# Performance work log

Measured on AMD Instinct MI355X. Metric: run time of the kernel, lower is better.

Reference implementation:

```python
import jax, jax.numpy as jnp
import numpy as np

E_NUM, R_NUM, DIM = 100000, 16, 32
BATCH, MAX_STEP, NEIGH, RULES = 1024, 2, 16, 8


def setup_inputs() -> dict:
    key = jax.random.key(0)
    ks = jax.random.split(key, 8)
    users = jax.random.randint(ks[0], (BATCH,), 0, E_NUM)
    items = jax.random.randint(ks[1], (BATCH,), 0, E_NUM)
    rules = jax.random.randint(ks[2], (RULES, MAX_STEP), 0, R_NUM)
    adj = jax.random.randint(ks[3], (R_NUM + 1, E_NUM, NEIGH), 0, E_NUM).astype(jnp.int32)
    ent_embed = jax.random.normal(ks[4], (E_NUM, DIM), jnp.float32) * 0.1
    rule_w = jax.random.normal(ks[5], (RULES,), jnp.float32) * 0.5
    W = jax.random.normal(ks[6], (DIM, 2 * DIM), jnp.float32) * (1.0 / np.sqrt(2 * DIM))
    b = jnp.zeros((DIM,), jnp.float32)
    return dict(users=users, items=items, rules=rules, adj=adj,
                ent_embed=ent_embed, rule_w=rule_w, W=W, b=b)


def _renorm(v, eps=1e-7):
    # emulate nn.Embedding(max_norm=1.0): clip row norms to <= 1 at lookup time
    n = jnp.linalg.norm(v, axis=-1, keepdims=True)
    return v * jnp.minimum(1.0, 1.0 / jnp.maximum(n, eps))


def reference(users, items, rules, adj, ent_embed, rule_w, W, b):
    B = users.shape[0]
    R, S = rules.shape
    N = adj.shape[2]
    dim = ent_embed.shape[1]

    # --- gather entity ids per hop: hop k has [B, R, N^k] (rule-major, as np.hstack) ---
    cur = jnp.broadcast_to(users[:, None], (B, R)).reshape(B, R, 1)
    hops = [cur.reshape(B, -1)]
    for s in range(S):
        rid = rules[:, s]                       # [R] relation id per rule at this step
        nxt = adj[rid[None, :, None], cur]      # [B, R, K, N]
        cur = nxt.reshape(B, R, -1)
        hops.append(cur.reshape(B, -1))

    # --- embed + max_norm renorm ---
    vecs = [_renorm(ent_embed[h]) for h in hops]  # hop k: [B, R*N^k, dim]

    # --- concat aggregator across hops (dropout p=0) ---
    for i in range(S):
        act = jnp.tanh if i == S - 1 else jax.nn.relu
        nxt_vecs = []
        for hop in range(S - i):
            selfv = vecs[hop]                                # [B, M, dim]
            neigh = vecs[hop + 1].reshape(B, -1, N, dim)     # [B, M, N, dim]
            h = jnp.concatenate([selfv, neigh.mean(axis=2)], axis=-1)  # [B, M, 2*dim]
            nxt_vecs.append(act(jnp.einsum('bmd,od->bmo', h, W) + b))
        vecs = nxt_vecs

    res = vecs[0].reshape(B, R, dim)             # per-rule user representation
    rw = _renorm(rule_w[None, :])[0]             # rule_embed with max_norm=1.0
    user_out = jnp.sum(res * rw[None, :, None], axis=1)      # [B, dim]
    item_emb = _renorm(ent_embed[items])                     # [B, dim]
    return jax.nn.sigmoid(jnp.sum(user_out * item_emb, axis=-1))  # [B]
```

## Files before the change

### kernel.cpp

```cpp
#include <hip/hip_runtime.h>
#include <hip/hip_fp16.h>
#include <math.h>

#define E_NUMC 100000
#define DIMC 32
#define NEIGHC 16
#define RULESC 8

struct __align__(16) h2x4 { __half2 x, y, z, w; };
struct __align__(8)  h2x2 { __half2 x, y; };

typedef _Float16 half8 __attribute__((ext_vector_type(8)));
typedef float    floatx4 __attribute__((ext_vector_type(4)));
typedef float    fx2 __attribute__((ext_vector_type(2)));

__global__ __launch_bounds__(256) void renorm_kernel(
    const float* __restrict__ emb, short* __restrict__ o8,
    const float* __restrict__ W, _Float16* __restrict__ Whg)
{
    if (blockIdx.x == 0) {
        const float4* W4 = (const float4*)W;
        const int o = threadIdx.x >> 3, oct = threadIdx.x & 7;
        const float4 wa = W4[o * 16 + 2 * oct];
        const float4 wb = W4[o * 16 + 2 * oct + 1];
        half8 hw;
        hw[0] = (_Float16)wa.x; hw[1] = (_Float16)wa.y;
        hw[2] = (_Float16)wa.z; hw[3] = (_Float16)wa.w;
        hw[4] = (_Float16)wb.x; hw[5] = (_Float16)wb.y;
        hw[6] = (_Float16)wb.z; hw[7] = (_Float16)wb.w;
        *(half8*)&Whg[o * 64 + 8 * oct] = hw;
    }
    const int row = blockIdx.x * 16 + (threadIdx.x >> 4);
    const int j = threadIdx.x & 15;
    const float2 f = ((const float2*)(emb + (long)row * DIMC))[j];
    float sq = f.x * f.x + f.y * f.y;
    sq += __shfl_xor(sq, 1, 64);
    sq += __shfl_xor(sq, 2, 64);
    sq += __shfl_xor(sq, 4, 64);
    sq += __shfl_xor(sq, 8, 64);
    const float s = fminf(1.0f, 1.0f / fmaxf(sqrtf(sq), 1e-7f));
    const int pk = __builtin_amdgcn_cvt_pk_fp8_f32(f.x * s, f.y * s, 0, false);
    o8[(long)row * (DIMC / 2) + j] = (short)(pk & 0xffff);
}

__global__ __launch_bounds__(256, 6) void rgrec_tree16_kernel(
    const int* __restrict__ users, const int* __restrict__ items,
    const int* __restrict__ rules, const int* __restrict__ adj,
    const float* __restrict__ emb, const uint2* __restrict__ emb8,
    const _Float16* __restrict__ Whg, const float* __restrict__ bvec,
    float* __restrict__ resS)
{
    const int b = blockIdx.x;
    const int r = blockIdx.y;
    const int t = threadIdx.x;
    const int lane = t & 63;
    const int wave = t >> 6;

    __shared__ _Float16 Xh[16][72];
    __shared__ _Float16 Wh[32][72];
    __shared__ _Float16 u16[72];
    __shared__ float mean1p[2][36];
    __shared__ float xe[68];
    __shared__ float bs[32];

    const int user = users[b];
    const int rid0 = rules[r * 2 + 0];
    const int rid1 = rules[r * 2 + 1];

    int h1v = 0;
    if (lane < 16) h1v = adj[(rid0 * E_NUMC + user) * NEIGHC + lane];

    float itv = 0.0f;
    if (t < 32) {
        const int it = items[b];
        itv = emb[(long)it * DIMC + t];
        float sq = itv * itv;
        sq += __shfl_xor(sq, 1, 64);
        sq += __shfl_xor(sq, 2, 64);
        sq += __shfl_xor(sq, 4, 64);
        sq += __shfl_xor(sq, 8, 64);
        sq += __shfl_xor(sq, 16, 64);
        itv *= fminf(1.0f, 1.0f / fmaxf(sqrtf(sq), 1e-7f));
    }

    const int m = t >> 4;
    const int j = t & 15;
    const int e1 = __shfl(h1v, m, 64);
    const int e2 = adj[(rid1 * E_NUMC + e1) * NEIGHC + j];

    const int g = t >> 3, k8 = t & 7;
    const bool cact = (t < 136);
    float4 craw = make_float4(0.f, 0.f, 0.f, 0.f);
    if (cact) {
        const int ec = (g < 16) ? __shfl(h1v, g, 64) : user;
        craw = ((const float4*)(emb + (long)ec * DIMC))[k8];
    }

    {
        const int o = t >> 3, oct = t & 7;
        *(half8*)&Wh[o][8 * oct] = *(const half8*)&Whg[o * 64 + 8 * oct];
    }
    if (t < 32) bs[t] = bvec[t];

    {
        const int k = j & 3;
        const int h = j >> 2;
        const int gbase = t & 48;
        float acc[8];
#pragma unroll
        for (int d = 0; d < 8; ++d) acc[d] = 0.0f;
#pragma unroll
        for (int i = 0; i < 4; ++i) {
            const int ec = __shfl(e2, gbase + h + 4 * i, 64);
            const uint2 v = emb8[(long)ec * 4 + k];
            const fx2 p0 = __builtin_amdgcn_cvt_pk_f32_fp8(v.x, false);
            const fx2 p1 = __builtin_amdgcn_cvt_pk_f32_fp8(v.x, true);
            const fx2 p2 = __builtin_amdgcn_cvt_pk_f32_fp8(v.y, false);
            const fx2 p3 = __builtin_amdgcn_cvt_pk_f32_fp8(v.y, true);
            acc[0] += p0[0]; acc[1] += p0[1];
            acc[2] += p1[0]; acc[3] += p1[1];
            acc[4] += p2[0]; acc[5] += p2[1];
            acc[6] += p3[0]; acc[7] += p3[1];
        }
#pragma unroll
        for (int d = 0; d < 8; ++d) acc[d] += __shfl_xor(acc[d], 4, 64);
#pragma unroll
        for (int d = 0; d < 8; ++d) acc[d] += __shfl_xor(acc[d], 8, 64);
        *(__half2*)&Xh[m][32 + 8 * k + 2 * h] =
            __floats2half2_rn(acc[2 * h] * (1.0f / 16.0f),
                              acc[2 * h + 1] * (1.0f / 16.0f));
    }

    if (cact) {
        float sq = craw.x * craw.x + craw.y * craw.y +
                   craw.z * craw.z + craw.w * craw.w;
        sq += __shfl_xor(sq, 1, 64);
        sq += __shfl_xor(sq, 2, 64);
        sq += __shfl_xor(sq, 4, 64);
        const float s = fminf(1.0f, 1.0f / fmaxf(sqrtf(sq), 1e-7f));
        const float c0 = craw.x * s, c1 = craw.y * s;
        const float c2 = craw.z * s, c3 = craw.w * s;
        const __half2 ha = __floats2half2_rn(c0, c1);
        const __half2 hb = __floats2half2_rn(c2, c3);
        if (g < 16) {
            *(__half2*)&Xh[g][4 * k8]     = ha;
            *(__half2*)&Xh[g][4 * k8 + 2] = hb;
        } else {
            *(__half2*)&u16[4 * k8]     = ha;
            *(__half2*)&u16[4 * k8 + 2] = hb;
        }
        if (t < 128) {
            float d0 = c0, d1 = c1, d2 = c2, d3 = c3;
#pragma unroll
            for (int st = 8; st <= 32; st <<= 1) {
                d0 += __shfl_xor(d0, st, 64);
                d1 += __shfl_xor(d1, st, 64);
                d2 += __shfl_xor(d2, st, 64);
                d3 += __shfl_xor(d3, st, 64);
            }
            if ((lane & 56) == 0)
                *(float4*)&mean1p[wave][4 * k8] = make_float4(d0, d1, d2, d3);
        }
    }
    __syncthreads();

    const int cn = lane & 15;
    const int kg = lane >> 4;
    if (wave < 2) {
        const half8 a0 = *(const half8*)&Xh[cn][8 * kg];
        const half8 a1 = *(const half8*)&Xh[cn][32 + 8 * kg];
        const half8 b0 = *(const half8*)&Wh[cn + 16 * wave][8 * kg];
        const half8 b1 = *(const half8*)&Wh[cn + 16 * wave][32 + 8 * kg];
        floatx4 acc = {0.0f, 0.0f, 0.0f, 0.0f};
        acc = __builtin_amdgcn_mfma_f32_16x16x32_f16(a0, b0, acc, 0, 0, 0);
        acc = __builtin_amdgcn_mfma_f32_16x16x32_f16(a1, b1, acc, 0, 0, 0);
        const float bb = bs[cn + 16 * wave];
        float csum = 0.0f;
#pragma unroll
        for (int q = 0; q < 4; ++q) csum += fmaxf(acc[q] + bb, 0.0f);
        csum += __shfl_xor(csum, 16, 64);
        csum += __shfl_xor(csum, 32, 64);
        if (lane < 16) xe[32 + cn + 16 * wave] = csum * (1.0f / 16.0f);
    } else if (wave == 2) {
        const int o = lane & 31, h = lane >> 5;
        float a = 0.0f;
        if (h == 0) {
#pragma unroll
            for (int oct = 0; oct < 4; ++oct) {
                const half8 u = *(const half8*)&u16[8 * oct];
                const half8 w = *(const half8*)&Wh[o][8 * oct];
#pragma unroll
                for (int q = 0; q < 8; ++q) a += (float)u[q] * (float)w[q];
            }
        } else {
#pragma unroll
            for (int oct = 0; oct < 4; ++oct) {
                const half8 w = *(const half8*)&Wh[o][32 + 8 * oct];
                const float4 p0a = *(const float4*)&mean1p[0][8 * oct];
                const float4 p0b = *(const float4*)&mean1p[0][8 * oct + 4];
                const float4 p1a = *(const float4*)&mean1p[1][8 * oct];
                const float4 p1b = *(const float4*)&mean1p[1][8 * oct + 4];
                a += (float)w[0] * (p0a.x + p1a.x) + (float)w[1] * (p0a.y + p1a.y)
                   + (float)w[2] * (p0a.z + p1a.z) + (float)w[3] * (p0a.w + p1a.w)
                   + (float)w[4] * (p0b.x + p1b.x) + (float)w[5] * (p0b.y + p1b.y)
                   + (float)w[6] * (p0b.z + p1b.z) + (float)w[7] * (p0b.w + p1b.w);
            }
            a *= (1.0f / 16.0f);
        }
        a += __shfl_xor(a, 32, 64);
        if (h == 0) xe[o] = fmaxf(a + bs[o], 0.0f);
    }
    __syncthreads();

    if (t < 64) {
        const int o = lane & 31, h = lane >> 5;
        float a = 0.0f;
#pragma unroll
        for (int oct = 4 * h; oct < 4 * h + 4; ++oct) {
            const half8 w = *(const half8*)&Wh[o][8 * oct];
            const float4 xa = *(const float4*)&xe[8 * oct];
            const float4 xb = *(const float4*)&xe[8 * oct + 4];
            a += (float)w[0] * xa.x + (float)w[1] * xa.y
               + (float)w[2] * xa.z + (float)w[3] * xa.w
               + (float)w[4] * xb.x + (float)w[5] * xb.y
               + (float)w[6] * xb.z + (float)w[7] * xb.w;
        }
        a += __shfl_xor(a, 32, 64);
        float p = (h == 0) ? tanhf(a + bs[o]) * itv : 0.0f;
        p += __shfl_xor(p, 1, 64);
        p += __shfl_xor(p, 2, 64);
        p += __shfl_xor(p, 4, 64);
        p += __shfl_xor(p, 8, 64);
        p += __shfl_xor(p, 16, 64);
        if (t == 0) resS[b * RULESC + r] = p;
    }
}

__global__ __launch_bounds__(256) void rgrec_sig_kernel(
    const float* __restrict__ rule_w, const float* __restrict__ resS,
    float* __restrict__ out, int B)
{
    const int b = blockIdx.x * 256 + threadIdx.x;
    if (b >= B) return;

    float ss = 0.0f;
    float rw[RULESC];
#pragma unroll
    for (int i = 0; i < RULESC; ++i) { rw[i] = rule_w[i]; ss += rw[i] * rw[i]; }
    const float rws = fminf(1.0f, 1.0f / fmaxf(sqrtf(ss), 1e-7f));

    const float4 r0 = ((const float4*)(resS + b * RULESC))[0];
    const float4 r1 = ((const float4*)(resS + b * RULESC))[1];
    const float acc = rw[0] * r0.x + rw[1] * r0.y + rw[2] * r0.z + rw[3] * r0.w
                    + rw[4] * r1.x + rw[5] * r1.y + rw[6] * r1.z + rw[7] * r1.w;
    out[b] = 1.0f / (1.0f + expf(-acc * rws));
}

__global__ __launch_bounds__(256) void rgrec_fused_kernel(
    const int* __restrict__ users, const int* __restrict__ items,
    const int* __restrict__ rules, const int* __restrict__ adj,
    const float* __restrict__ emb, const float* __restrict__ rule_w,
    const float* __restrict__ W, const float* __restrict__ bvec,
    float* __restrict__ out)
{
    const int b = blockIdx.x;
    const int t = threadIdx.x;

    __shared__ float Wt[64][33];
    __shared__ float bs[32];
    __shared__ float h1s[16][33];
    __shared__ float mean2[16][33];
    __shared__ float v1[16][33];
    __shared__ float u_vec[32];
    __shared__ float mean1[32];
    __shared__ float v0[32];
    __shared__ float meanv1[32];
    __shared__ float useru[32];
    __shared__ int   h1id[16];

    for (int i = t; i < 64 * 32; i += 256) {
        const int o = i >> 6, d = i & 63;
        Wt[d][o] = W[i];
    }
    if (t < 32) { bs[t] = bvec[t]; useru[t] = 0.0f; }

    float ss = 0.0f;
#pragma unroll
    for (int i = 0; i < RULESC; ++i) { const float w = rule_w[i]; ss += w * w; }
    const float rws = fminf(1.0f, 1.0f / fmaxf(sqrtf(ss), 1e-7f));

    const int user = users[b];

    for (int r = 0; r < RULESC; ++r) {
        const int rid0 = rules[r * 2 + 0];
        const int rid1 = rules[r * 2 + 1];
        if (t < 16) h1id[t] = adj[(rid0 * E_NUMC + user) * NEIGHC + t];
        __syncthreads();
        {
            const int m = t >> 4, j = t & 15;
            const int e1 = h1id[m];
            const int e2 = adj[(rid1 * E_NUMC + e1) * NEIGHC + j];
            float v[32];
            const float4* p = (const float4*)(emb + (long)e2 * DIMC);
            float sq = 0.0f;
#pragma unroll
            for (int q = 0; q < 8; ++q) {
                const float4 f = p[q];
                v[q * 4 + 0] = f.x; v[q * 4 + 1] = f.y;
                v[q * 4 + 2] = f.z; v[q * 4 + 3] = f.w;
                sq += f.x * f.x + f.y * f.y + f.z * f.z + f.w * f.w;
            }
            const float s =
                fminf(1.0f, 1.0f / fmaxf(sqrtf(sq), 1e-7f)) * (1.0f / 16.0f);
#pragma unroll
            for (int d = 0; d < 32; ++d) v[d] *= s;
#pragma unroll
            for (int st = 1; st < 16; st <<= 1) {
#pragma unroll
                for (int d = 0; d < 32; ++d) v[d] += __shfl_xor(v[d], st, 64);
            }
            mean2[m][j]      = v[j];
            mean2[m][j + 16] = v[j + 16];
        }
        if (t < 136) {
            const int g = t >> 3, k = t & 7;
            const int e = (g < 16) ? h1id[g] : user;
            const float4 f = ((const float4*)(emb + (long)e * DIMC))[k];
            float sq = f.x * f.x + f.y * f.y + f.z * f.z + f.w * f.w;
            sq += __shfl_xor(sq, 1, 64);
            sq += __shfl_xor(sq, 2, 64);
            sq += __shfl_xor(sq, 4, 64);
            const float s = fminf(1.0f, 1.0f / fmaxf(sqrtf(sq), 1e-7f));
            if (g < 16) {
                h1s[g][k * 4 + 0] = f.x * s; h1s[g][k * 4 + 1] = f.y * s;
                h1s[g][k * 4 + 2] = f.z * s; h1s[g][k * 4 + 3] = f.w * s;
            } else {
                u_vec[k * 4 + 0] = f.x * s; u_vec[k * 4 + 1] = f.y * s;
                u_vec[k * 4 + 2] = f.z * s; u_vec[k * 4 + 3] = f.w * s;
            }
        }
        __syncthreads();
        {
            const int m = t >> 4, o = t & 15;
            float a0 = bs[o], a1 = bs[o + 16];
#pragma unroll
            for (int d = 0; d < 32; ++d) {
                const float h = h1s[m][d];
                a0 += Wt[d][o] * h;
                a1 += Wt[d][o + 16] * h;
            }
#pragma unroll
            for (int d = 0; d < 32; ++d) {
                const float h = mean2[m][d];
                a0 += Wt[32 + d][o] * h;
                a1 += Wt[32 + d][o + 16] * h;
            }
            v1[m][o]      = fmaxf(a0, 0.0f);
            v1[m][o + 16] = fmaxf(a1, 0.0f);
        }
        if (t < 32) {
            float mn = 0.0f;
#pragma unroll
            for (int m2 = 0; m2 < 16; ++m2) mn += h1s[m2][t];
            mean1[t] = mn * (1.0f / 16.0f);
        }
        __syncthreads();
        if (t < 32) {
            float a = bs[t];
#pragma unroll
            for (int d = 0; d < 32; ++d) a += Wt[d][t] * u_vec[d];
#pragma unroll
            for (int d = 0; d < 32; ++d) a += Wt[32 + d][t] * mean1[d];
            v0[t] = fmaxf(a, 0.0f);
            float mv = 0.0f;
#pragma unroll
            for (int m2 = 0; m2 < 16; ++m2) mv += v1[m2][t];
            meanv1[t] = mv * (1.0f / 16.0f);
        }
        __syncthreads();
        if (t < 32) {
            float a = bs[t];
#pragma unroll
            for (int d = 0; d < 32; ++d) a += Wt[d][t] * v0[d];
#pragma unroll
            for (int d = 0; d < 32; ++d) a += Wt[32 + d][t] * meanv1[d];
            useru[t] += rule_w[r] * rws * tanhf(a);
        }
        __syncthreads();
    }

    if (t < 32) {
        const int it = items[b];
        const float x = emb[(long)it * DIMC + t];
        float sq = x * x;
        sq += __shfl_xor(sq, 1, 64);
        sq += __shfl_xor(sq, 2, 64);
        sq += __shfl_xor(sq, 4, 64);
        sq += __shfl_xor(sq, 8, 64);
        sq += __shfl_xor(sq, 16, 64);
        const float s = fminf(1.0f, 1.0f / fmaxf(sqrtf(sq), 1e-7f));
        float p = useru[t] * x * s;
        p += __shfl_xor(p, 1, 64);
        p += __shfl_xor(p, 2, 64);
        p += __shfl_xor(p, 4, 64);
        p += __shfl_xor(p, 8, 64);
        p += __shfl_xor(p, 16, 64);
        if (t == 0) out[b] = 1.0f / (1.0f + expf(-p));
    }
}

extern "C" void kernel_launch(void* const* d_in, const int* in_sizes, int n_in,
                              void* d_out, int out_size, void* d_ws, size_t ws_size,
                              hipStream_t stream) {
    const int*   users  = (const int*)d_in[0];
    const int*   items  = (const int*)d_in[1];
    const int*   rules  = (const int*)d_in[2];
    const int*   adj    = (const int*)d_in[3];
    const float* emb    = (const float*)d_in[4];
    const float* rule_w = (const float*)d_in[5];
    const float* W      = (const float*)d_in[6];
    const float* bvec   = (const float*)d_in[7];
    float*       out    = (float*)d_out;

    const int batch = in_sizes[0];
    const size_t emb8_bytes = (size_t)E_NUMC * DIMC;
    const size_t whg_bytes  = (size_t)DIMC * 2 * DIMC * sizeof(short);
    const size_t res_bytes  = (size_t)batch * RULESC * sizeof(float);

    if (ws_size >= emb8_bytes + whg_bytes + res_bytes) {
        short*    emb8s = (short*)d_ws;
        _Float16* whg   = (_Float16*)((char*)d_ws + emb8_bytes);
        float*    resS  = (float*)((char*)d_ws + emb8_bytes + whg_bytes);

        renorm_kernel<<<dim3(E_NUMC / 16), dim3(256), 0, stream>>>(
            emb, emb8s, W, whg);
        rgrec_tree16_kernel<<<dim3(batch, RULESC), dim3(256), 0, stream>>>(
            users, items, rules, adj, emb, (const uint2*)emb8s, whg, bvec, resS);
        rgrec_sig_kernel<<<dim3((batch + 255) / 256), dim3(256), 0, stream>>>(
            rule_w, resS, out, batch);
    } else {
        rgrec_fused_kernel<<<dim3(batch), dim3(256), 0, stream>>>(
            users, items, rules, adj, emb, rule_w, W, bvec, out);
    }
}
```

Baseline: 39.91 us.

## Map one rule per wave, remove block barriers, read weights from global

Restructures the tree kernel so that each wave handles one (user, rule) pair and each block covers four rules. The grid shrinks from batch×8 to batch×2 and no __syncthreads barriers remain. Each wave now gathers all 16×16 second-hop fp8 embeddings itself, using int4 adjacency loads and 8 batched loads per pass. It also computes the first-hop mean with shuffles and runs the MFMA for both output halves. Weights and bias are read directly from global or cache instead of being staged in LDS. The aim is to cut block-level sync and the launch count, at the cost of more per-wave serial work and repeated global weight loads.

```diff
diff --git a/kernel.cpp b/kernel.cpp
--- a/kernel.cpp
+++ b/kernel.cpp
@@ -43,7 +43,7 @@
     o8[(long)row * (DIMC / 2) + j] = (short)(pk & 0xffff);
 }
 
-__global__ __launch_bounds__(256, 6) void rgrec_tree16_kernel(
+__global__ __launch_bounds__(256, 8) void rgrec_tree1w_kernel(
     const int* __restrict__ users, const int* __restrict__ items,
     const int* __restrict__ rules, const int* __restrict__ adj,
     const float* __restrict__ emb, const uint2* __restrict__ emb8,
@@ -51,17 +51,13 @@
     float* __restrict__ resS)
 {
     const int b = blockIdx.x;
-    const int r = blockIdx.y;
     const int t = threadIdx.x;
+    const int wave = t >> 6;
     const int lane = t & 63;
-    const int wave = t >> 6;
-
-    __shared__ _Float16 Xh[16][72];
-    __shared__ _Float16 Wh[32][72];
-    __shared__ _Float16 u16[72];
-    __shared__ float mean1p[2][36];
-    __shared__ float xe[68];
-    __shared__ float bs[32];
+    const int r = blockIdx.y * 4 + wave;
+
+    __shared__ _Float16 Xh[4][17][72];
+    __shared__ float    xe[4][68];
 
     const int user = users[b];
     const int rid0 = rules[r * 2 + 0];
@@ -70,10 +66,14 @@
     int h1v = 0;
     if (lane < 16) h1v = adj[(rid0 * E_NUMC + user) * NEIGHC + lane];
 
-    float itv = 0.0f;
-    if (t < 32) {
+    const int m = lane >> 2, q = lane & 3;
+    const int e1m = __shfl(h1v, m, 64);
+    const int4 e2q = ((const int4*)(adj + ((long)rid1 * E_NUMC + e1m) * NEIGHC))[q];
+
+    float itv;
+    {
         const int it = items[b];
-        itv = emb[(long)it * DIMC + t];
+        itv = emb[(long)it * DIMC + (lane & 31)];
         float sq = itv * itv;
         sq += __shfl_xor(sq, 1, 64);
         sq += __shfl_xor(sq, 2, 64);
@@ -83,156 +83,134 @@
         itv *= fminf(1.0f, 1.0f / fmaxf(sqrtf(sq), 1e-7f));
     }
 
-    const int m = t >> 4;
-    const int j = t & 15;
-    const int e1 = __shfl(h1v, m, 64);
-    const int e2 = adj[(rid1 * E_NUMC + e1) * NEIGHC + j];
-
-    const int g = t >> 3, k8 = t & 7;
-    const bool cact = (t < 136);
-    float4 craw = make_float4(0.f, 0.f, 0.f, 0.f);
-    if (cact) {
-        const int ec = (g < 16) ? __shfl(h1v, g, 64) : user;
-        craw = ((const float4*)(emb + (long)ec * DIMC))[k8];
-    }
-
-    {
-        const int o = t >> 3, oct = t & 7;
-        *(half8*)&Wh[o][8 * oct] = *(const half8*)&Whg[o * 64 + 8 * oct];
-    }
-    if (t < 32) bs[t] = bvec[t];
-
-    {
-        const int k = j & 3;
-        const int h = j >> 2;
-        const int gbase = t & 48;
+    const float sc = 1.0f / 16.0f;
+    {
         float acc[8];
 #pragma unroll
         for (int d = 0; d < 8; ++d) acc[d] = 0.0f;
 #pragma unroll
-        for (int i = 0; i < 4; ++i) {
-            const int ec = __shfl(e2, gbase + h + 4 * i, 64);
-            const uint2 v = emb8[(long)ec * 4 + k];
-            const fx2 p0 = __builtin_amdgcn_cvt_pk_f32_fp8(v.x, false);
-            const fx2 p1 = __builtin_amdgcn_cvt_pk_f32_fp8(v.x, true);
-            const fx2 p2 = __builtin_amdgcn_cvt_pk_f32_fp8(v.y, false);
-            const fx2 p3 = __builtin_amdgcn_cvt_pk_f32_fp8(v.y, true);
-            acc[0] += p0[0]; acc[1] += p0[1];
-            acc[2] += p1[0]; acc[3] += p1[1];
-            acc[4] += p2[0]; acc[5] += p2[1];
-            acc[6] += p3[0]; acc[7] += p3[1];
-        }
-#pragma unroll
-        for (int d = 0; d < 8; ++d) acc[d] += __shfl_xor(acc[d], 4, 64);
-#pragma unroll
-        for (int d = 0; d < 8; ++d) acc[d] += __shfl_xor(acc[d], 8, 64);
-        *(__half2*)&Xh[m][32 + 8 * k + 2 * h] =
-            __floats2half2_rn(acc[2 * h] * (1.0f / 16.0f),
-                              acc[2 * h + 1] * (1.0f / 16.0f));
-    }
-
-    if (cact) {
-        float sq = craw.x * craw.x + craw.y * craw.y +
-                   craw.z * craw.z + craw.w * craw.w;
-        sq += __shfl_xor(sq, 1, 64);
-        sq += __shfl_xor(sq, 2, 64);
-        sq += __shfl_xor(sq, 4, 64);
-        const float s = fminf(1.0f, 1.0f / fmaxf(sqrtf(sq), 1e-7f));
-        const float c0 = craw.x * s, c1 = craw.y * s;
-        const float c2 = craw.z * s, c3 = craw.w * s;
-        const __half2 ha = __floats2half2_rn(c0, c1);
-        const __half2 hb = __floats2half2_rn(c2, c3);
-        if (g < 16) {
-            *(__half2*)&Xh[g][4 * k8]     = ha;
-            *(__half2*)&Xh[g][4 * k8 + 2] = hb;
-        } else {
-            *(__half2*)&u16[4 * k8]     = ha;
-            *(__half2*)&u16[4 * k8 + 2] = hb;
-        }
-        if (t < 128) {
-            float d0 = c0, d1 = c1, d2 = c2, d3 = c3;
-#pragma unroll
-            for (int st = 8; st <= 32; st <<= 1) {
-                d0 += __shfl_xor(d0, st, 64);
-                d1 += __shfl_xor(d1, st, 64);
-                d2 += __shfl_xor(d2, st, 64);
-                d3 += __shfl_xor(d3, st, 64);
-            }
-            if ((lane & 56) == 0)
-                *(float4*)&mean1p[wave][4 * k8] = make_float4(d0, d1, d2, d3);
-        }
-    }
-    __syncthreads();
-
-    const int cn = lane & 15;
-    const int kg = lane >> 4;
-    if (wave < 2) {
-        const half8 a0 = *(const half8*)&Xh[cn][8 * kg];
-        const half8 a1 = *(const half8*)&Xh[cn][32 + 8 * kg];
-        const half8 b0 = *(const half8*)&Wh[cn + 16 * wave][8 * kg];
-        const half8 b1 = *(const half8*)&Wh[cn + 16 * wave][32 + 8 * kg];
-        floatx4 acc = {0.0f, 0.0f, 0.0f, 0.0f};
-        acc = __builtin_amdgcn_mfma_f32_16x16x32_f16(a0, b0, acc, 0, 0, 0);
-        acc = __builtin_amdgcn_mfma_f32_16x16x32_f16(a1, b1, acc, 0, 0, 0);
-        const float bb = bs[cn + 16 * wave];
-        float csum = 0.0f;
-#pragma unroll
-        for (int q = 0; q < 4; ++q) csum += fmaxf(acc[q] + bb, 0.0f);
-        csum += __shfl_xor(csum, 16, 64);
-        csum += __shfl_xor(csum, 32, 64);
-        if (lane < 16) xe[32 + cn + 16 * wave] = csum * (1.0f / 16.0f);
-    } else if (wave == 2) {
-        const int o = lane & 31, h = lane >> 5;
+        for (int half = 0; half < 2; ++half) {
+            uint2 vb[8];
+#pragma unroll
+            for (int s = 0; s < 8; ++s) {
+                const int c = half * 8 + s;
+                const int comp = c & 3;
+                const int src = (m << 2) + (c >> 2);
+                const int ec = __shfl(comp == 0 ? e2q.x : comp == 1 ? e2q.y :
+                                      comp == 2 ? e2q.z : e2q.w, src, 64);
+                vb[s] = emb8[(long)ec * 4 + q];
+            }
+#pragma unroll
+            for (int s = 0; s < 8; ++s) {
+                const fx2 p0 = __builtin_amdgcn_cvt_pk_f32_fp8(vb[s].x, false);
+                const fx2 p1 = __builtin_amdgcn_cvt_pk_f32_fp8(vb[s].x, true);
+                const fx2 p2 = __builtin_amdgcn_cvt_pk_f32_fp8(vb[s].y, false);
+                const fx2 p3 = __builtin_amdgcn_cvt_pk_f32_fp8(vb[s].y, true);
+                acc[0] += p0[0]; acc[1] += p0[1];
+                acc[2] += p1[0]; acc[3] += p1[1];
+                acc[4] += p2[0]; acc[5] += p2[1];
+                acc[6] += p3[0]; acc[7] += p3[1];
+            }
+        }
+        h2x4 st;
+        st.x = __floats2half2_rn(acc[0] * sc, acc[1] * sc);
+        st.y = __floats2half2_rn(acc[2] * sc, acc[3] * sc);
+        st.z = __floats2half2_rn(acc[4] * sc, acc[5] * sc);
+        st.w = __floats2half2_rn(acc[6] * sc, acc[7] * sc);
+        *(h2x4*)&Xh[wave][m][32 + 8 * q] = st;
+    }
+
+    {
+        const int k8 = lane & 7;
+        float ps0 = 0.f, ps1 = 0.f, ps2 = 0.f, ps3 = 0.f;
+#pragma unroll
+        for (int it3 = 0; it3 < 3; ++it3) {
+            const int g2 = it3 * 8 + (lane >> 3);
+            const int eh = __shfl(h1v, g2 & 15, 64);
+            if (g2 <= 16) {
+                const int e = (g2 < 16) ? eh : user;
+                const float4 f = ((const float4*)(emb + (long)e * DIMC))[k8];
+                float sq = f.x * f.x + f.y * f.y + f.z * f.z + f.w * f.w;
+                sq += __shfl_xor(sq, 1, 64);
+                sq += __shfl_xor(sq, 2, 64);
+                sq += __shfl_xor(sq, 4, 64);
+                const float s = fminf(1.0f, 1.0f / fmaxf(sqrtf(sq), 1e-7f));
+                const float c0 = f.x * s, c1 = f.y * s;
+                const float c2 = f.z * s, c3 = f.w * s;
+                *(__half2*)&Xh[wave][g2][4 * k8]     = __floats2half2_rn(c0, c1);
+                *(__half2*)&Xh[wave][g2][4 * k8 + 2] = __floats2half2_rn(c2, c3);
+                if (g2 < 16) { ps0 += c0; ps1 += c1; ps2 += c2; ps3 += c3; }
+            }
+        }
+        ps0 += __shfl_xor(ps0, 8, 64);  ps1 += __shfl_xor(ps1, 8, 64);
+        ps2 += __shfl_xor(ps2, 8, 64);  ps3 += __shfl_xor(ps3, 8, 64);
+        ps0 += __shfl_xor(ps0, 16, 64); ps1 += __shfl_xor(ps1, 16, 64);
+        ps2 += __shfl_xor(ps2, 16, 64); ps3 += __shfl_xor(ps3, 16, 64);
+        ps0 += __shfl_xor(ps0, 32, 64); ps1 += __shfl_xor(ps1, 32, 64);
+        ps2 += __shfl_xor(ps2, 32, 64); ps3 += __shfl_xor(ps3, 32, 64);
+        if (lane < 8) {
+            *(__half2*)&Xh[wave][16][32 + 4 * k8] =
+                __floats2half2_rn(ps0 * sc, ps1 * sc);
+            *(__half2*)&Xh[wave][16][32 + 4 * k8 + 2] =
+                __floats2half2_rn(ps2 * sc, ps3 * sc);
+        }
+    }
+
+    const int cn = lane & 15, kg = lane >> 4;
+    {
+        const half8 a0 = *(const half8*)&Xh[wave][cn][8 * kg];
+        const half8 a1 = *(const half8*)&Xh[wave][cn][32 + 8 * kg];
+#pragma unroll
+        for (int nh = 0; nh < 2; ++nh) {
+            const half8 b0 = *(const half8*)&Whg[(cn + 16 * nh) * 64 + 8 * kg];
+            const half8 b1 = *(const half8*)&Whg[(cn + 16 * nh) * 64 + 32 + 8 * kg];
+            floatx4 acc4 = {0.0f, 0.0f, 0.0f, 0.0f};
+            acc4 = __builtin_amdgcn_mfma_f32_16x16x32_f16(a0, b0, acc4, 0, 0, 0);
+            acc4 = __builtin_amdgcn_mfma_f32_16x16x32_f16(a1, b1, acc4, 0, 0, 0);
+            const float bb = bvec[cn + 16 * nh];
+            float cs = 0.0f;
+#pragma unroll
+            for (int e = 0; e < 4; ++e) cs += fmaxf(acc4[e] + bb, 0.0f);
+            cs += __shfl_xor(cs, 16, 64);
+            cs += __shfl_xor(cs, 32, 64);
+            if (lane < 16) xe[wave][32 + cn + 16 * nh] = cs * sc;
+        }
+    }
+
+    const int o = lane & 31, hh = lane >> 5;
+    {
         float a = 0.0f;
-        if (h == 0) {
-#pragma unroll
-            for (int oct = 0; oct < 4; ++oct) {
-                const half8 u = *(const half8*)&u16[8 * oct];
-                const half8 w = *(const half8*)&Wh[o][8 * oct];
-#pragma unroll
-                for (int q = 0; q < 8; ++q) a += (float)u[q] * (float)w[q];
-            }
-        } else {
-#pragma unroll
-            for (int oct = 0; oct < 4; ++oct) {
-                const half8 w = *(const half8*)&Wh[o][32 + 8 * oct];
-                const float4 p0a = *(const float4*)&mean1p[0][8 * oct];
-                const float4 p0b = *(const float4*)&mean1p[0][8 * oct + 4];
-                const float4 p1a = *(const float4*)&mean1p[1][8 * oct];
-                const float4 p1b = *(const float4*)&mean1p[1][8 * oct + 4];
-                a += (float)w[0] * (p0a.x + p1a.x) + (float)w[1] * (p0a.y + p1a.y)
-                   + (float)w[2] * (p0a.z + p1a.z) + (float)w[3] * (p0a.w + p1a.w)
-                   + (float)w[4] * (p0b.x + p1b.x) + (float)w[5] * (p0b.y + p1b.y)
-                   + (float)w[6] * (p0b.z + p1b.z) + (float)w[7] * (p0b.w + p1b.w);
-            }
-            a *= (1.0f / 16.0f);
+#pragma unroll
+        for (int oct = 4 * hh; oct < 4 * hh + 4; ++oct) {
+            const half8 u = *(const half8*)&Xh[wave][16][8 * oct];
+            const half8 w = *(const half8*)&Whg[o * 64 + 8 * oct];
+#pragma unroll
+            for (int e = 0; e < 8; ++e) a += (float)u[e] * (float)w[e];
         }
         a += __shfl_xor(a, 32, 64);
-        if (h == 0) xe[o] = fmaxf(a + bs[o], 0.0f);
-    }
-    __syncthreads();
-
-    if (t < 64) {
-        const int o = lane & 31, h = lane >> 5;
+        if (hh == 0) xe[wave][o] = fmaxf(a + bvec[o], 0.0f);
+    }
+
+    {
         float a = 0.0f;
 #pragma unroll
-        for (int oct = 4 * h; oct < 4 * h + 4; ++oct) {
-            const half8 w = *(const half8*)&Wh[o][8 * oct];
-            const float4 xa = *(const float4*)&xe[8 * oct];
-            const float4 xb = *(const float4*)&xe[8 * oct + 4];
+        for (int oct = 4 * hh; oct < 4 * hh + 4; ++oct) {
+            const half8 w = *(const half8*)&Whg[o * 64 + 8 * oct];
+            const float4 xa = *(const float4*)&xe[wave][8 * oct];
+            const float4 xb = *(const float4*)&xe[wave][8 * oct + 4];
             a += (float)w[0] * xa.x + (float)w[1] * xa.y
                + (float)w[2] * xa.z + (float)w[3] * xa.w
                + (float)w[4] * xb.x + (float)w[5] * xb.y
                + (float)w[6] * xb.z + (float)w[7] * xb.w;
         }
         a += __shfl_xor(a, 32, 64);
-        float p = (h == 0) ? tanhf(a + bs[o]) * itv : 0.0f;
+        float p = (hh == 0) ? tanhf(a + bvec[o]) * itv : 0.0f;
         p += __shfl_xor(p, 1, 64);
         p += __shfl_xor(p, 2, 64);
         p += __shfl_xor(p, 4, 64);
         p += __shfl_xor(p, 8, 64);
         p += __shfl_xor(p, 16, 64);
-        if (t == 0) resS[b * RULESC + r] = p;
+        if (lane == 0) resS[b * RULESC + r] = p;
     }
 }
 
@@ -434,7 +412,7 @@
 
         renorm_kernel<<<dim3(E_NUMC / 16), dim3(256), 0, stream>>>(
             emb, emb8s, W, whg);
-        rgrec_tree16_kernel<<<dim3(batch, RULESC), dim3(256), 0, stream>>>(
+        rgrec_tree1w_kernel<<<dim3(batch, 2), dim3(256), 0, stream>>>(
             users, items, rules, adj, emb, (const uint2*)emb8s, whg, bvec, resS);
         rgrec_sig_kernel<<<dim3((batch + 255) / 256), dim3(256), 0, stream>>>(
             rule_w, resS, out, batch);
```

Result: slower. 41.01 us (+2.7%).
